# Kernel tuning notes

Measured on AMD Instinct MI355X. Metric: run time of the kernel, lower is better.

Reference implementation:

```python
import jax, jax.numpy as jnp
import numpy as np

N = 50000
E = 400000
F_IN = 128
NUM_CLASSES = 16
# (heads, out_channels, concat) per GATConv layer
LAYERS = [(8, 32, True), (8, 16, True), (8, 8, True), (1, NUM_CLASSES, False)]
DIMS_IN = [F_IN, 256, 128, 64]
NEG_SLOPE = 0.2
BN_EPS = 1e-5


def setup_inputs() -> dict:
    key = jax.random.key(0)
    ks = iter(jax.random.split(key, 64))
    inp = {}
    inp["x"] = jax.random.normal(next(ks), (N, F_IN), dtype=jnp.float32)
    inp["src"] = jax.random.randint(next(ks), (E,), 0, N, dtype=jnp.int32)
    inp["dst"] = jax.random.randint(next(ks), (E,), 0, N, dtype=jnp.int32)
    for l, ((h, c, concat), din) in enumerate(zip(LAYERS, DIMS_IN), start=1):
        s = 1.0 / np.sqrt(din)
        inp[f"W{l}"] = jax.random.normal(next(ks), (din, h * c), dtype=jnp.float32) * s
        inp[f"asrc{l}"] = jax.random.normal(next(ks), (h, c), dtype=jnp.float32) * 0.1
        inp[f"adst{l}"] = jax.random.normal(next(ks), (h, c), dtype=jnp.float32) * 0.1
        dout = h * c if concat else c
        inp[f"b{l}"] = jax.random.normal(next(ks), (dout,), dtype=jnp.float32) * 0.01
        inp[f"g{l}"] = jax.random.uniform(next(ks), (dout,), dtype=jnp.float32, minval=0.5, maxval=1.5)
        inp[f"be{l}"] = jax.random.normal(next(ks), (dout,), dtype=jnp.float32) * 0.1
        inp[f"rm{l}"] = jax.random.normal(next(ks), (dout,), dtype=jnp.float32) * 0.1
        inp[f"rv{l}"] = jax.random.uniform(next(ks), (dout,), dtype=jnp.float32, minval=0.5, maxval=1.5)
    return inp


def _gat_conv(x, src, dst, W, a_src, a_dst, bias, heads, ch, concat):
    n = x.shape[0]
    h = (x @ W).reshape(n, heads, ch)                     # [N,H,C]
    e_s = jnp.einsum('nhc,hc->nh', h, a_src)              # [N,H]
    e_d = jnp.einsum('nhc,hc->nh', h, a_dst)
    alpha = jax.nn.leaky_relu(e_s[src] + e_d[dst], NEG_SLOPE)   # [E,H]
    amax = jax.ops.segment_max(alpha, dst, num_segments=n)
    ex = jnp.exp(alpha - amax[dst])
    den = jax.ops.segment_sum(ex, dst, num_segments=n)
    attn = ex / (den[dst] + 1e-16)                        # [E,H]
    out = jax.ops.segment_sum(h[src] * attn[:, :, None], dst, num_segments=n)  # [N,H,C]
    out = out.reshape(n, heads * ch) if concat else out.mean(axis=1)
    return out + bias


def _bn(x, g, b, rm, rv):
    return (x - rm) * jax.lax.rsqrt(rv + BN_EPS) * g + b


def _forward(x, src, dst, params):
    # PyG GATConv adds self-loops by default
    loops = jnp.arange(N, dtype=src.dtype)
    s = jnp.concatenate([src, loops])
    d = jnp.concatenate([dst, loops])
    out = x
    for l, (h, c, concat) in enumerate(LAYERS, start=1):
        W, a_s, a_d, b, g, be, rm, rv = (params[f"{k}{l}"] for k in
                                         ("W", "asrc", "adst", "b", "g", "be", "rm", "rv"))
        out = _gat_conv(out, s, d, W, a_s, a_d, b, h, c, concat)
        if l < 4:
            out = jax.nn.elu(out)
        out = _bn(out, g, be, rm, rv)
    return out


def reference(x, src, dst,
              W1, asrc1, adst1, b1, g1, be1, rm1, rv1,
              W2, asrc2, adst2, b2, g2, be2, rm2, rv2,
              W3, asrc3, adst3, b3, g3, be3, rm3, rv3,
              W4, asrc4, adst4, b4, g4, be4, rm4, rv4):
    params = dict(
        W1=W1, asrc1=asrc1, adst1=adst1, b1=b1, g1=g1, be1=be1, rm1=rm1, rv1=rv1,
        W2=W2, asrc2=asrc2, adst2=adst2, b2=b2, g2=g2, be2=be2, rm2=rm2, rv2=rv2,
        W3=W3, asrc3=asrc3, adst3=adst3, b3=b3, g3=g3, be3=be3, rm3=rm3, rv3=rv3,
        W4=W4, asrc4=asrc4, adst4=adst4, b4=b4, g4=g4, be4=be4, rm4=rm4, rv4=rv4)
    return _forward(x, src, dst, params)
```

## Files before the change

### kernel.cpp

```cpp
#include <hip/hip_runtime.h>

#define NEG_SLOPE 0.2f
#define BN_EPS 1e-5f

typedef unsigned short u16;
typedef unsigned int u32;
typedef __bf16 bf16x8 __attribute__((ext_vector_type(8)));
typedef float f32x4 __attribute__((ext_vector_type(4)));

__device__ __forceinline__ u32 f2bf(float f) {
    u32 u = __float_as_uint(f);
    return (u + 0x7FFFu + ((u >> 16) & 1u)) >> 16;
}
__device__ __forceinline__ float bf2f(u32 h) { return __uint_as_float(h << 16); }
__device__ __forceinline__ float bfl(u32 p) { return __uint_as_float(p << 16); }
__device__ __forceinline__ float bfh(u32 p) { return __uint_as_float(p & 0xFFFF0000u); }

__global__ void split_kernel(const float4* __restrict__ X, uint2* __restrict__ hi,
                             uint2* __restrict__ lo, int n4) {
    int i = blockIdx.x * blockDim.x + threadIdx.x;
    if (i >= n4) return;
    float4 v = X[i];
    u32 h0 = f2bf(v.x), h1 = f2bf(v.y), h2 = f2bf(v.z), h3 = f2bf(v.w);
    hi[i] = make_uint2(h0 | (h1 << 16), h2 | (h3 << 16));
    u32 l0 = f2bf(v.x - bf2f(h0)), l1 = f2bf(v.y - bf2f(h1)),
        l2 = f2bf(v.z - bf2f(h2)), l3 = f2bf(v.w - bf2f(h3));
    lo[i] = make_uint2(l0 | (l1 << 16), l2 | (l3 << 16));
}

__global__ void wt_prep(const float* __restrict__ W, u16* __restrict__ hi,
                        u16* __restrict__ lo, int K, int N) {
    int i = blockIdx.x * blockDim.x + threadIdx.x;
    if (i >= K * N) return;
    int k = i / N, n = i - k * N;
    float w = W[i];
    u32 h = f2bf(w);
    hi[n * K + k] = (u16)h;
    lo[n * K + k] = (u16)f2bf(w - bf2f(h));
}

__launch_bounds__(256)
__global__ void gemm_mfma(const u16* __restrict__ Ahi, const u16* __restrict__ Alo,
                          const u16* __restrict__ Bhi, const u16* __restrict__ Blo,
                          u16* __restrict__ Cbf, int M, int K, int N) {
    __shared__ uint4 sA[2][512];
    __shared__ uint4 sB[2][512];
    const int tid = threadIdx.x;
    const int bm = blockIdx.y * 128;
    const int bn = blockIdx.x * 128;
    const int lane = tid & 63;
    const int w = tid >> 6;
    const int wm = (w >> 1) * 64;
    const int wn = (w & 1) * 64;
    const int fr = lane & 15;
    const int fs = lane >> 4;
    f32x4 zero = {0.f, 0.f, 0.f, 0.f};
    f32x4 acc[4][4];
    #pragma unroll
    for (int i = 0; i < 4; i++)
        #pragma unroll
        for (int j = 0; j < 4; j++) acc[i][j] = zero;

    const int r0 = tid >> 2;
    const int ss = tid & 3;
    const int r1 = r0 + 64;
    const int d0 = r0 * 4 + (ss ^ ((r0 >> 1) & 3));
    const int d1 = r1 * 4 + (ss ^ ((r1 >> 1) & 3));

    for (int k0 = 0; k0 < K; k0 += 32) {
        {
            int gr = bm + r0;
            uint4 vh = make_uint4(0, 0, 0, 0), vl = make_uint4(0, 0, 0, 0);
            if (gr < M) {
                vh = *(const uint4*)(Ahi + (size_t)gr * K + k0 + ss * 8);
                vl = *(const uint4*)(Alo + (size_t)gr * K + k0 + ss * 8);
            }
            sA[0][d0] = vh; sA[1][d0] = vl;
            gr = bm + r1;
            vh = make_uint4(0, 0, 0, 0); vl = make_uint4(0, 0, 0, 0);
            if (gr < M) {
                vh = *(const uint4*)(Ahi + (size_t)gr * K + k0 + ss * 8);
                vl = *(const uint4*)(Alo + (size_t)gr * K + k0 + ss * 8);
            }
            sA[0][d1] = vh; sA[1][d1] = vl;
        }
        {
            int gr = bn + r0;
            sB[0][d0] = *(const uint4*)(Bhi + (size_t)gr * K + k0 + ss * 8);
            sB[1][d0] = *(const uint4*)(Blo + (size_t)gr * K + k0 + ss * 8);
            gr = bn + r1;
            sB[0][d1] = *(const uint4*)(Bhi + (size_t)gr * K + k0 + ss * 8);
            sB[1][d1] = *(const uint4*)(Blo + (size_t)gr * K + k0 + ss * 8);
        }
        __syncthreads();
        bf16x8 ah[4], al[4], bh[4], bl[4];
        #pragma unroll
        for (int mi = 0; mi < 4; mi++) {
            int row = wm + mi * 16 + fr;
            int idx = row * 4 + (fs ^ ((row >> 1) & 3));
            ah[mi] = *reinterpret_cast<const bf16x8*>(&sA[0][idx]);
            al[mi] = *reinterpret_cast<const bf16x8*>(&sA[1][idx]);
        }
        #pragma unroll
        for (int ni = 0; ni < 4; ni++) {
            int row = wn + ni * 16 + fr;
            int idx = row * 4 + (fs ^ ((row >> 1) & 3));
            bh[ni] = *reinterpret_cast<const bf16x8*>(&sB[0][idx]);
            bl[ni] = *reinterpret_cast<const bf16x8*>(&sB[1][idx]);
        }
        #pragma unroll
        for (int mi = 0; mi < 4; mi++)
            #pragma unroll
            for (int ni = 0; ni < 4; ni++) {
                acc[mi][ni] = __builtin_amdgcn_mfma_f32_16x16x32_bf16(ah[mi], bh[ni], acc[mi][ni], 0, 0, 0);
                acc[mi][ni] = __builtin_amdgcn_mfma_f32_16x16x32_bf16(ah[mi], bl[ni], acc[mi][ni], 0, 0, 0);
                acc[mi][ni] = __builtin_amdgcn_mfma_f32_16x16x32_bf16(al[mi], bh[ni], acc[mi][ni], 0, 0, 0);
            }
        __syncthreads();
    }
    #pragma unroll
    for (int mi = 0; mi < 4; mi++) {
        #pragma unroll
        for (int ni = 0; ni < 4; ni++) {
            int colg = bn + wn + ni * 16 + fr;
            int rbase = bm + wm + mi * 16 + fs * 4;
            #pragma unroll
            for (int r = 0; r < 4; r++) {
                int rw = rbase + r;
                if (rw < M) Cbf[(size_t)rw * N + colg] = (u16)f2bf(acc[mi][ni][r]);
            }
        }
    }
}

template<int TN>
__launch_bounds__(256)
__global__ void gemm_tile(const float* __restrict__ A, const float* __restrict__ B,
                          u16* __restrict__ Cbf, int M, int K, int N) {
    constexpr int BNt = 16 * TN;
    __shared__ float As[32][132];
    __shared__ float Bs[32][BNt + 4];
    const int bm = blockIdx.y * 128;
    const int bn = blockIdx.x * BNt;
    const int tid = threadIdx.x;
    const int tr = tid >> 4;
    const int tc = tid & 15;
    const int la_m = tid >> 3;
    const int la_k = (tid & 7) << 2;
    const int lb_row = tid / (BNt / 4);
    const int lb_c = (tid % (BNt / 4)) * 4;
    float acc[8][TN] = {};
    for (int k0 = 0; k0 < K; k0 += 32) {
        #pragma unroll
        for (int p = 0; p < 4; p++) {
            int m = la_m + p * 32;
            int gm = bm + m;
            float4 v = make_float4(0.f, 0.f, 0.f, 0.f);
            if (gm < M) v = *reinterpret_cast<const float4*>(&A[(size_t)gm * K + k0 + la_k]);
            As[la_k + 0][m] = v.x;
            As[la_k + 1][m] = v.y;
            As[la_k + 2][m] = v.z;
            As[la_k + 3][m] = v.w;
        }
        #pragma unroll
        for (int p = 0; p < BNt / 32; p++) {
            int kk = lb_row + p * (1024 / BNt);
            *reinterpret_cast<float4*>(&Bs[kk][lb_c]) =
                *reinterpret_cast<const float4*>(&B[(size_t)(k0 + kk) * N + bn + lb_c]);
        }
        __syncthreads();
        #pragma unroll
        for (int kk = 0; kk < 32; kk++) {
            float a[8], b[TN];
            float4 a0 = *reinterpret_cast<const float4*>(&As[kk][tr * 4]);
            float4 a1 = *reinterpret_cast<const float4*>(&As[kk][64 + tr * 4]);
            a[0] = a0.x; a[1] = a0.y; a[2] = a0.z; a[3] = a0.w;
            a[4] = a1.x; a[5] = a1.y; a[6] = a1.z; a[7] = a1.w;
            float4 b0 = *reinterpret_cast<const float4*>(&Bs[kk][tc * 4]);
            b[0] = b0.x; b[1] = b0.y; b[2] = b0.z; b[3] = b0.w;
            if constexpr (TN == 8) {
                float4 b1 = *reinterpret_cast<const float4*>(&Bs[kk][64 + tc * 4]);
                b[4] = b1.x; b[5] = b1.y; b[6] = b1.z; b[7] = b1.w;
            }
            #pragma unroll
            for (int i = 0; i < 8; i++)
                #pragma unroll
                for (int j = 0; j < TN; j++)
                    acc[i][j] += a[i] * b[j];
        }
        __syncthreads();
    }
    #pragma unroll
    for (int i = 0; i < 8; i++) {
        int m = bm + ((i < 4) ? (tr * 4 + i) : (64 + tr * 4 + (i - 4)));
        if (m >= M) continue;
        uint2 p0 = make_uint2(f2bf(acc[i][0]) | (f2bf(acc[i][1]) << 16),
                              f2bf(acc[i][2]) | (f2bf(acc[i][3]) << 16));
        *reinterpret_cast<uint2*>(&Cbf[(size_t)m * N + bn + tc * 4]) = p0;
        if constexpr (TN == 8) {
            uint2 p1 = make_uint2(f2bf(acc[i][4]) | (f2bf(acc[i][5]) << 16),
                                  f2bf(acc[i][6]) | (f2bf(acc[i][7]) << 16));
            *reinterpret_cast<uint2*>(&Cbf[(size_t)m * N + bn + 64 + tc * 4]) = p1;
        }
    }
}

__launch_bounds__(256)
__global__ void gemm_k64n16(const float* __restrict__ A, const float* __restrict__ B,
                            u16* __restrict__ Cbf, int M) {
    __shared__ float As[64][68];
    __shared__ float Bs[64][16];
    const int tid = threadIdx.x;
    const int bm = blockIdx.x * 64;
    {
        int r = tid >> 2, c = (tid & 3) << 2;
        *reinterpret_cast<float4*>(&Bs[r][c]) = *reinterpret_cast<const float4*>(&B[r * 16 + c]);
    }
    #pragma unroll
    for (int p = 0; p < 4; p++) {
        int m = (tid >> 4) + p * 16;
        int c = (tid & 15) << 2;
        int gm = bm + m;
        float4 v = make_float4(0.f, 0.f, 0.f, 0.f);
        if (gm < M) v = *reinterpret_cast<const float4*>(&A[(size_t)gm * 64 + c]);
        *reinterpret_cast<float4*>(&As[m][c]) = v;
    }
    __syncthreads();
    const int tc = tid & 15;
    const int r0 = tid >> 4;
    float acc[4] = {};
    #pragma unroll
    for (int k4 = 0; k4 < 16; k4++) {
        float b0 = Bs[4 * k4 + 0][tc];
        float b1 = Bs[4 * k4 + 1][tc];
        float b2 = Bs[4 * k4 + 2][tc];
        float b3 = Bs[4 * k4 + 3][tc];
        #pragma unroll
        for (int i = 0; i < 4; i++) {
            float4 av = *reinterpret_cast<const float4*>(&As[r0 + i * 16][4 * k4]);
            acc[i] += av.x * b0 + av.y * b1 + av.z * b2 + av.w * b3;
        }
    }
    #pragma unroll
    for (int i = 0; i < 4; i++) {
        int m = bm + r0 + i * 16;
        if (m < M) Cbf[(size_t)m * 16 + tc] = (u16)f2bf(acc[i]);
    }
}

__global__ void scores_kernel(const u16* __restrict__ h,
                              const float* __restrict__ asrc,
                              const float* __restrict__ adst,
                              float* __restrict__ es, float* __restrict__ ed,
                              int Nn, int H, int C) {
    int idx = blockIdx.x * blockDim.x + threadIdx.x;
    if (idx >= Nn * H) return;
    int n = idx / H, hh = idx % H;
    const u16* hp = h + ((size_t)n * H + hh) * C;
    const float4* ap = reinterpret_cast<const float4*>(asrc + hh * C);
    const float4* bp = reinterpret_cast<const float4*>(adst + hh * C);
    float s = 0.f, d = 0.f;
    for (int c4 = 0; c4 < C / 4; c4++) {
        uint2 pv = *reinterpret_cast<const uint2*>(hp + 4 * c4);
        float v0 = bfl(pv.x), v1 = bfh(pv.x), v2 = bfl(pv.y), v3 = bfh(pv.y);
        float4 a = ap[c4], b = bp[c4];
        s += v0 * a.x + v1 * a.y + v2 * a.z + v3 * a.w;
        d += v0 * b.x + v1 * b.y + v2 * b.z + v3 * b.w;
    }
    es[idx] = s;
    ed[idx] = d;
}

__global__ void hist_kernel(const int* __restrict__ dst, int* __restrict__ counts,
                            int E0, int Etot) {
    int e = blockIdx.x * blockDim.x + threadIdx.x;
    if (e >= Etot) return;
    int d_ = (e < E0) ? dst[e] : e - E0;
    atomicAdd(&counts[d_], 1);
}

__global__ void scan_kernel(const int* __restrict__ counts, int* __restrict__ row_ptr, int Nn) {
    __shared__ int wsum[16];
    __shared__ int chunk_total;
    __shared__ int carry_s;
    const int tid = threadIdx.x;
    const int lane = tid & 63;
    const int wid = tid >> 6;
    if (tid == 0) carry_s = 0;
    __syncthreads();
    for (int base = 0; base < Nn; base += 1024) {
        int i = base + tid;
        int v = (i < Nn) ? counts[i] : 0;
        int iv = v;
        #pragma unroll
        for (int off = 1; off < 64; off <<= 1) {
            int t = __shfl_up(iv, off, 64);
            if (lane >= off) iv += t;
        }
        if (lane == 63) wsum[wid] = iv;
        __syncthreads();
        if (tid == 0) {
            int s = 0;
            #pragma unroll
            for (int k = 0; k < 16; k++) { int t = wsum[k]; wsum[k] = s; s += t; }
            chunk_total = s;
        }
        __syncthreads();
        if (i < Nn) row_ptr[i] = carry_s + wsum[wid] + (iv - v);
        __syncthreads();
        if (tid == 0) carry_s += chunk_total;
        __syncthreads();
    }
    if (tid == 0) row_ptr[Nn] = carry_s;
}

__global__ void scatter_kernel(const int* __restrict__ src, const int* __restrict__ dst,
                               int* __restrict__ cursor, int* __restrict__ col,
                               int E0, int Etot) {
    int e = blockIdx.x * blockDim.x + threadIdx.x;
    if (e >= Etot) return;
    int d_ = (e < E0) ? dst[e] : e - E0;
    int s_ = (e < E0) ? src[e] : e - E0;
    int pos = atomicAdd(&cursor[d_], 1);
    col[pos] = s_;
}

template<int H, int C, int NT, int DO_ELU>
__launch_bounds__(256)
__global__ void gat_fused(const int* __restrict__ row_ptr, const int* __restrict__ col,
                          const float* __restrict__ es, const float* __restrict__ ed,
                          const u16* __restrict__ h16, float* __restrict__ out,
                          const float* __restrict__ bias, const float* __restrict__ g,
                          const float* __restrict__ be, const float* __restrict__ rm,
                          const float* __restrict__ rv, int Nn) {
    constexpr int Dout = H * C;
    constexpr int VEC = Dout / NT;
    constexpr int NPB = 256 / NT;
    constexpr int CH = 64;
    __shared__ float w_s[NPB][CH][H];
    __shared__ int   c_s[NPB][CH];
    __shared__ float ed_s[NPB][H];
    __shared__ int   md;
    const int tid = threadIdx.x;
    const int slot = tid / NT;
    const int t = tid % NT;
    const int node = blockIdx.x * NPB + slot;
    const bool alive = node < Nn;
    int jb = 0, je = 0;
    if (alive) { jb = row_ptr[node]; je = row_ptr[node + 1]; }
    if (tid == 0) md = 0;
    __syncthreads();
    if (alive && t == 0) atomicMax(&md, je - jb);
    if (alive && t < H) ed_s[slot][t] = ed[node * H + t];
    __syncthreads();
    const int nch = (md + CH - 1) / CH;
    const int c0 = t * VEC;
    const int hh = c0 / C;
    float acc[VEC] = {};
    float den = 0.f;
    for (int cc = 0; cc < nch; cc++) {
        int j0 = jb + cc * CH;
        int cnt = je - j0;
        if (cnt > CH) cnt = CH;
        if (alive) {
            for (int tt = t; tt < cnt; tt += NT) {
                int s = col[j0 + tt];
                c_s[slot][tt] = s;
                if constexpr (H == 8) {
                    const float4* ep = reinterpret_cast<const float4*>(&es[s * 8]);
                    float4 e0 = ep[0], e1 = ep[1];
                    float al[8] = {e0.x, e0.y, e0.z, e0.w, e1.x, e1.y, e1.z, e1.w};
                    #pragma unroll
                    for (int h2 = 0; h2 < 8; h2++) {
                        float a = al[h2] + ed_s[slot][h2];
                        a = (a >= 0.f) ? a : NEG_SLOPE * a;
                        w_s[slot][tt][h2] = __expf(a);
                    }
                } else {
                    float a = es[s] + ed_s[slot][0];
                    a = (a >= 0.f) ? a : NEG_SLOPE * a;
                    w_s[slot][tt][0] = __expf(a);
                }
            }
        }
        __syncthreads();
        if (alive && cnt > 0) {
            int j = 0;
            if constexpr (VEC == 4) {
                for (; j + 4 <= cnt; j += 4) {
                    int s0 = c_s[slot][j],     s1 = c_s[slot][j + 1];
                    int s2 = c_s[slot][j + 2], s3 = c_s[slot][j + 3];
                    float w0 = w_s[slot][j][hh],     w1 = w_s[slot][j + 1][hh];
                    float w2 = w_s[slot][j + 2][hh], w3 = w_s[slot][j + 3][hh];
                    const uint2 p0 = *reinterpret_cast<const uint2*>(h16 + (size_t)s0 * Dout + c0);
                    const uint2 p1 = *reinterpret_cast<const uint2*>(h16 + (size_t)s1 * Dout + c0);
                    const uint2 p2 = *reinterpret_cast<const uint2*>(h16 + (size_t)s2 * Dout + c0);
                    const uint2 p3 = *reinterpret_cast<const uint2*>(h16 + (size_t)s3 * Dout + c0);
                    den += (w0 + w1) + (w2 + w3);
                    acc[0] += w0 * bfl(p0.x) + w1 * bfl(p1.x) + w2 * bfl(p2.x) + w3 * bfl(p3.x);
                    acc[1] += w0 * bfh(p0.x) + w1 * bfh(p1.x) + w2 * bfh(p2.x) + w3 * bfh(p3.x);
                    acc[2] += w0 * bfl(p0.y) + w1 * bfl(p1.y) + w2 * bfl(p2.y) + w3 * bfl(p3.y);
                    acc[3] += w0 * bfh(p0.y) + w1 * bfh(p1.y) + w2 * bfh(p2.y) + w3 * bfh(p3.y);
                }
            } else if constexpr (VEC == 2) {
                for (; j + 4 <= cnt; j += 4) {
                    int s0 = c_s[slot][j],     s1 = c_s[slot][j + 1];
                    int s2 = c_s[slot][j + 2], s3 = c_s[slot][j + 3];
                    float w0 = w_s[slot][j][hh],     w1 = w_s[slot][j + 1][hh];
                    float w2 = w_s[slot][j + 2][hh], w3 = w_s[slot][j + 3][hh];
                    const u32 p0 = *reinterpret_cast<const u32*>(h16 + (size_t)s0 * Dout + c0);
                    const u32 p1 = *reinterpret_cast<const u32*>(h16 + (size_t)s1 * Dout + c0);
                    const u32 p2 = *reinterpret_cast<const u32*>(h16 + (size_t)s2 * Dout + c0);
                    const u32 p3 = *reinterpret_cast<const u32*>(h16 + (size_t)s3 * Dout + c0);
                    den += (w0 + w1) + (w2 + w3);
                    acc[0] += w0 * bfl(p0) + w1 * bfl(p1) + w2 * bfl(p2) + w3 * bfl(p3);
                    acc[1] += w0 * bfh(p0) + w1 * bfh(p1) + w2 * bfh(p2) + w3 * bfh(p3);
                }
            } else {
                for (; j + 4 <= cnt; j += 4) {
                    int s0 = c_s[slot][j],     s1 = c_s[slot][j + 1];
                    int s2 = c_s[slot][j + 2], s3 = c_s[slot][j + 3];
                    float w0 = w_s[slot][j][hh],     w1 = w_s[slot][j + 1][hh];
                    float w2 = w_s[slot][j + 2][hh], w3 = w_s[slot][j + 3][hh];
                    float v0 = bf2f(h16[(size_t)s0 * Dout + c0]);
                    float v1 = bf2f(h16[(size_t)s1 * Dout + c0]);
                    float v2 = bf2f(h16[(size_t)s2 * Dout + c0]);
                    float v3 = bf2f(h16[(size_t)s3 * Dout + c0]);
                    den += (w0 + w1) + (w2 + w3);
                    acc[0] += w0 * v0 + w1 * v1 + w2 * v2 + w3 * v3;
                }
            }
            for (; j < cnt; j++) {
                float w = w_s[slot][j][hh];
                den += w;
                const u16* hp = h16 + (size_t)c_s[slot][j] * Dout + c0;
                if constexpr (VEC == 4) {
                    const uint2 pv = *reinterpret_cast<const uint2*>(hp);
                    acc[0] += w * bfl(pv.x); acc[1] += w * bfh(pv.x);
                    acc[2] += w * bfl(pv.y); acc[3] += w * bfh(pv.y);
                } else if constexpr (VEC == 2) {
                    const u32 pv = *reinterpret_cast<const u32*>(hp);
                    acc[0] += w * bfl(pv); acc[1] += w * bfh(pv);
                } else {
                    acc[0] += w * bf2f(hp[0]);
                }
            }
        }
        __syncthreads();
    }
    if (!alive) return;
    const float inv = 1.f / (den + 1e-16f);
    float res[VEC];
    #pragma unroll
    for (int v = 0; v < VEC; v++) {
        const int jc = c0 + v;
        float y = acc[v] * inv + bias[jc];
        if (DO_ELU) y = (y > 0.f) ? y : expm1f(y);
        y = (y - rm[jc]) * rsqrtf(rv[jc] + BN_EPS) * g[jc] + be[jc];
        res[v] = y;
    }
    float* op = out + (size_t)node * Dout + c0;
    if constexpr (VEC == 4) {
        *reinterpret_cast<float4*>(op) = make_float4(res[0], res[1], res[2], res[3]);
    } else if constexpr (VEC == 2) {
        *reinterpret_cast<float2*>(op) = make_float2(res[0], res[1]);
    } else {
        op[0] = res[0];
    }
}

extern "C" void kernel_launch(void* const* d_in, const int* in_sizes, int n_in,
                              void* d_out, int out_size, void* d_ws, size_t ws_size,
                              hipStream_t stream) {
    const float* x = (const float*)d_in[0];
    const int* src = (const int*)d_in[1];
    const int* dst = (const int*)d_in[2];
    const int Nn = in_sizes[0] / 128;
    const int E0 = in_sizes[1];
    const int Etot = E0 + Nn;

    float* B0 = (float*)d_ws;
    float* B1 = B0 + (size_t)Nn * 256;
    float* es = B1 + (size_t)Nn * 256;
    float* ed = es + (size_t)Nn * 8;
    int* row_ptr = (int*)(ed + (size_t)Nn * 8);
    int* cursor  = row_ptr + (Nn + 1);
    int* col     = cursor + Nn;
    u16* wth = (u16*)(col + Etot);
    u16* wtl = wth + 256 * 256;

    hipMemsetAsync(cursor, 0, sizeof(int) * Nn, stream);
    hist_kernel<<<(Etot + 255) / 256, 256, 0, stream>>>(dst, cursor, E0, Etot);
    scan_kernel<<<1, 1024, 0, stream>>>(cursor, row_ptr, Nn);
    hipMemcpyAsync(cursor, row_ptr, sizeof(int) * Nn, hipMemcpyDeviceToDevice, stream);
    scatter_kernel<<<(Etot + 255) / 256, 256, 0, stream>>>(src, dst, cursor, col, E0, Etot);

    const int gy128 = (Nn + 127) / 128;

    for (int l = 0; l < 4; l++) {
        const float* const* p = (const float* const*)(d_in + 3 + l * 8);
        const float* W    = p[0];
        const float* asrc = p[1];
        const float* adst = p[2];
        const float* bias = p[3];
        const float* g    = p[4];
        const float* be   = p[5];
        const float* rm   = p[6];
        const float* rv   = p[7];

        if (l == 0) {
            const int K = 128, N = 256;
            u16* SH = (u16*)B1;
            u16* SL = SH + (size_t)Nn * K;
            int n4 = Nn * K / 4;
            split_kernel<<<(n4 + 255) / 256, 256, 0, stream>>>(
                (const float4*)x, (uint2*)SH, (uint2*)SL, n4);
            wt_prep<<<(K * N + 255) / 256, 256, 0, stream>>>(W, wth, wtl, K, N);
            u16* h1 = (u16*)B0;
            gemm_mfma<<<dim3(N / 128, gy128), 256, 0, stream>>>(SH, SL, wth, wtl, h1, Nn, K, N);
            scores_kernel<<<(Nn * 8 + 255) / 256, 256, 0, stream>>>(h1, asrc, adst, es, ed, Nn, 8, 32);
            gat_fused<8, 32, 64, 1><<<(Nn + 3) / 4, 256, 0, stream>>>(
                row_ptr, col, es, ed, h1, B1, bias, g, be, rm, rv, Nn);
        } else if (l == 1) {
            const int K = 256, N = 128;
            u16* SH = (u16*)B0;
            u16* SL = SH + (size_t)Nn * K;
            int n4 = Nn * K / 4;
            split_kernel<<<(n4 + 255) / 256, 256, 0, stream>>>(
                (const float4*)B1, (uint2*)SH, (uint2*)SL, n4);
            wt_prep<<<(K * N + 255) / 256, 256, 0, stream>>>(W, wth, wtl, K, N);
            u16* h2 = (u16*)B1;
            float* out2 = B1 + (size_t)Nn * 64;
            gemm_mfma<<<dim3(N / 128, gy128), 256, 0, stream>>>(SH, SL, wth, wtl, h2, Nn, K, N);
            scores_kernel<<<(Nn * 8 + 255) / 256, 256, 0, stream>>>(h2, asrc, adst, es, ed, Nn, 8, 16);
            gat_fused<8, 16, 64, 1><<<(Nn + 3) / 4, 256, 0, stream>>>(
                row_ptr, col, es, ed, h2, out2, bias, g, be, rm, rv, Nn);
        } else if (l == 2) {
            const float* in = B1 + (size_t)Nn * 64;
            u16* h3 = (u16*)B0;
            float* out3 = B0 + (size_t)Nn * 32;
            gemm_tile<4><<<dim3(1, gy128), 256, 0, stream>>>(in, W, h3, Nn, 128, 64);
            scores_kernel<<<(Nn * 8 + 255) / 256, 256, 0, stream>>>(h3, asrc, adst, es, ed, Nn, 8, 8);
            gat_fused<8, 8, 64, 1><<<(Nn + 3) / 4, 256, 0, stream>>>(
                row_ptr, col, es, ed, h3, out3, bias, g, be, rm, rv, Nn);
        } else {
            const float* in = B0 + (size_t)Nn * 32;
            u16* h4 = (u16*)B1;
            gemm_k64n16<<<(Nn + 63) / 64, 256, 0, stream>>>(in, W, h4, Nn);
            scores_kernel<<<(Nn + 255) / 256, 256, 0, stream>>>(h4, asrc, adst, es, ed, Nn, 1, 16);
            gat_fused<1, 16, 16, 0><<<(Nn + 15) / 16, 256, 0, stream>>>(
                row_ptr, col, es, ed, h4, (float*)d_out, bias, g, be, rm, rv, Nn);
        }
    }
}
```

Before: 407.1 us.

## Fuse bf16 hi/lo split into GAT epilogue, use MFMA for layer 3, widen per-thread vectors

The aggregation kernel now writes its outputs directly as bf16 hi/lo pairs, so the separate split pass before the next layer's GEMM is removed. Layer 3 moves from the scalar FP32 tiled GEMM to a BN=64 variant of the MFMA GEMM. The gather kernel gives each thread more features per node (8- or 4-wide loads) and packs more nodes per block. It drops the block-wide max-degree synchronization and __syncthreads, relying on per-wave LDS waits and early exit for dead nodes. This removes barrier stalls and an extra memory pass, at the cost of relying on wave-synchronous behaviour that only holds if each node's threads stay within one wavefront.

```diff
diff --git a/kernel.cpp b/kernel.cpp
--- a/kernel.cpp
+++ b/kernel.cpp
@@ -39,25 +39,27 @@
     lo[n * K + k] = (u16)f2bf(w - bf2f(h));
 }
 
+template<int BN>
 __launch_bounds__(256)
 __global__ void gemm_mfma(const u16* __restrict__ Ahi, const u16* __restrict__ Alo,
                           const u16* __restrict__ Bhi, const u16* __restrict__ Blo,
                           u16* __restrict__ Cbf, int M, int K, int N) {
+    constexpr int FM = (BN == 128) ? 4 : 2;
     __shared__ uint4 sA[2][512];
-    __shared__ uint4 sB[2][512];
+    __shared__ uint4 sB[2][BN * 4];
     const int tid = threadIdx.x;
     const int bm = blockIdx.y * 128;
-    const int bn = blockIdx.x * 128;
+    const int bn = blockIdx.x * BN;
     const int lane = tid & 63;
     const int w = tid >> 6;
-    const int wm = (w >> 1) * 64;
-    const int wn = (w & 1) * 64;
+    const int wm = (BN == 128) ? (w >> 1) * 64 : w * 32;
+    const int wn = (BN == 128) ? (w & 1) * 64 : 0;
     const int fr = lane & 15;
     const int fs = lane >> 4;
     f32x4 zero = {0.f, 0.f, 0.f, 0.f};
-    f32x4 acc[4][4];
-    #pragma unroll
-    for (int i = 0; i < 4; i++)
+    f32x4 acc[FM][4];
+    #pragma unroll
+    for (int i = 0; i < FM; i++)
         #pragma unroll
         for (int j = 0; j < 4; j++) acc[i][j] = zero;
 
@@ -88,14 +90,16 @@
             int gr = bn + r0;
             sB[0][d0] = *(const uint4*)(Bhi + (size_t)gr * K + k0 + ss * 8);
             sB[1][d0] = *(const uint4*)(Blo + (size_t)gr * K + k0 + ss * 8);
-            gr = bn + r1;
-            sB[0][d1] = *(const uint4*)(Bhi + (size_t)gr * K + k0 + ss * 8);
-            sB[1][d1] = *(const uint4*)(Blo + (size_t)gr * K + k0 + ss * 8);
-        }
-        __syncthreads();
-        bf16x8 ah[4], al[4], bh[4], bl[4];
-        #pragma unroll
-        for (int mi = 0; mi < 4; mi++) {
+            if constexpr (BN == 128) {
+                gr = bn + r1;
+                sB[0][d1] = *(const uint4*)(Bhi + (size_t)gr * K + k0 + ss * 8);
+                sB[1][d1] = *(const uint4*)(Blo + (size_t)gr * K + k0 + ss * 8);
+            }
+        }
+        __syncthreads();
+        bf16x8 ah[FM], al[FM], bh[4], bl[4];
+        #pragma unroll
+        for (int mi = 0; mi < FM; mi++) {
             int row = wm + mi * 16 + fr;
             int idx = row * 4 + (fs ^ ((row >> 1) & 3));
             ah[mi] = *reinterpret_cast<const bf16x8*>(&sA[0][idx]);
@@ -109,7 +113,7 @@
             bl[ni] = *reinterpret_cast<const bf16x8*>(&sB[1][idx]);
         }
         #pragma unroll
-        for (int mi = 0; mi < 4; mi++)
+        for (int mi = 0; mi < FM; mi++)
             #pragma unroll
             for (int ni = 0; ni < 4; ni++) {
                 acc[mi][ni] = __builtin_amdgcn_mfma_f32_16x16x32_bf16(ah[mi], bh[ni], acc[mi][ni], 0, 0, 0);
@@ -119,7 +123,7 @@
         __syncthreads();
     }
     #pragma unroll
-    for (int mi = 0; mi < 4; mi++) {
+    for (int mi = 0; mi < FM; mi++) {
         #pragma unroll
         for (int ni = 0; ni < 4; ni++) {
             int colg = bn + wn + ni * 16 + fr;
@@ -129,78 +133,6 @@
                 int rw = rbase + r;
                 if (rw < M) Cbf[(size_t)rw * N + colg] = (u16)f2bf(acc[mi][ni][r]);
             }
-        }
-    }
-}
-
-template<int TN>
-__launch_bounds__(256)
-__global__ void gemm_tile(const float* __restrict__ A, const float* __restrict__ B,
-                          u16* __restrict__ Cbf, int M, int K, int N) {
-    constexpr int BNt = 16 * TN;
-    __shared__ float As[32][132];
-    __shared__ float Bs[32][BNt + 4];
-    const int bm = blockIdx.y * 128;
-    const int bn = blockIdx.x * BNt;
-    const int tid = threadIdx.x;
-    const int tr = tid >> 4;
-    const int tc = tid & 15;
-    const int la_m = tid >> 3;
-    const int la_k = (tid & 7) << 2;
-    const int lb_row = tid / (BNt / 4);
-    const int lb_c = (tid % (BNt / 4)) * 4;
-    float acc[8][TN] = {};
-    for (int k0 = 0; k0 < K; k0 += 32) {
-        #pragma unroll
-        for (int p = 0; p < 4; p++) {
-            int m = la_m + p * 32;
-            int gm = bm + m;
-            float4 v = make_float4(0.f, 0.f, 0.f, 0.f);
-            if (gm < M) v = *reinterpret_cast<const float4*>(&A[(size_t)gm * K + k0 + la_k]);
-            As[la_k + 0][m] = v.x;
-            As[la_k + 1][m] = v.y;
-            As[la_k + 2][m] = v.z;
-            As[la_k + 3][m] = v.w;
-        }
-        #pragma unroll
-        for (int p = 0; p < BNt / 32; p++) {
-            int kk = lb_row + p * (1024 / BNt);
-            *reinterpret_cast<float4*>(&Bs[kk][lb_c]) =
-                *reinterpret_cast<const float4*>(&B[(size_t)(k0 + kk) * N + bn + lb_c]);
-        }
-        __syncthreads();
-        #pragma unroll
-        for (int kk = 0; kk < 32; kk++) {
-            float a[8], b[TN];
-            float4 a0 = *reinterpret_cast<const float4*>(&As[kk][tr * 4]);
-            float4 a1 = *reinterpret_cast<const float4*>(&As[kk][64 + tr * 4]);
-            a[0] = a0.x; a[1] = a0.y; a[2] = a0.z; a[3] = a0.w;
-            a[4] = a1.x; a[5] = a1.y; a[6] = a1.z; a[7] = a1.w;
-            float4 b0 = *reinterpret_cast<const float4*>(&Bs[kk][tc * 4]);
-            b[0] = b0.x; b[1] = b0.y; b[2] = b0.z; b[3] = b0.w;
-            if constexpr (TN == 8) {
-                float4 b1 = *reinterpret_cast<const float4*>(&Bs[kk][64 + tc * 4]);
-                b[4] = b1.x; b[5] = b1.y; b[6] = b1.z; b[7] = b1.w;
-            }
-            #pragma unroll
-            for (int i = 0; i < 8; i++)
-                #pragma unroll
-                for (int j = 0; j < TN; j++)
-                    acc[i][j] += a[i] * b[j];
-        }
-        __syncthreads();
-    }
-    #pragma unroll
-    for (int i = 0; i < 8; i++) {
-        int m = bm + ((i < 4) ? (tr * 4 + i) : (64 + tr * 4 + (i - 4)));
-        if (m >= M) continue;
-        uint2 p0 = make_uint2(f2bf(acc[i][0]) | (f2bf(acc[i][1]) << 16),
-                              f2bf(acc[i][2]) | (f2bf(acc[i][3]) << 16));
-        *reinterpret_cast<uint2*>(&Cbf[(size_t)m * N + bn + tc * 4]) = p0;
-        if constexpr (TN == 8) {
-            uint2 p1 = make_uint2(f2bf(acc[i][4]) | (f2bf(acc[i][5]) << 16),
-                                  f2bf(acc[i][6]) | (f2bf(acc[i][7]) << 16));
-            *reinterpret_cast<uint2*>(&Cbf[(size_t)m * N + bn + 64 + tc * 4]) = p1;
         }
     }
 }
@@ -325,130 +257,112 @@
     col[pos] = s_;
 }
 
-template<int H, int C, int NT, int DO_ELU>
+template<int H, int C, int NT, int DO_ELU, int OUT_HILO>
 __launch_bounds__(256)
 __global__ void gat_fused(const int* __restrict__ row_ptr, const int* __restrict__ col,
                           const float* __restrict__ es, const float* __restrict__ ed,
-                          const u16* __restrict__ h16, float* __restrict__ out,
+                          const u16* __restrict__ h16, float* __restrict__ outf,
+                          u16* __restrict__ outh, u16* __restrict__ outl,
                           const float* __restrict__ bias, const float* __restrict__ g,
                           const float* __restrict__ be, const float* __restrict__ rm,
                           const float* __restrict__ rv, int Nn) {
     constexpr int Dout = H * C;
     constexpr int VEC = Dout / NT;
     constexpr int NPB = 256 / NT;
-    constexpr int CH = 64;
+    constexpr int CH = 32;
     __shared__ float w_s[NPB][CH][H];
     __shared__ int   c_s[NPB][CH];
-    __shared__ float ed_s[NPB][H];
-    __shared__ int   md;
     const int tid = threadIdx.x;
     const int slot = tid / NT;
     const int t = tid % NT;
     const int node = blockIdx.x * NPB + slot;
-    const bool alive = node < Nn;
-    int jb = 0, je = 0;
-    if (alive) { jb = row_ptr[node]; je = row_ptr[node + 1]; }
-    if (tid == 0) md = 0;
-    __syncthreads();
-    if (alive && t == 0) atomicMax(&md, je - jb);
-    if (alive && t < H) ed_s[slot][t] = ed[node * H + t];
-    __syncthreads();
-    const int nch = (md + CH - 1) / CH;
+    if (node >= Nn) return;
+    const int jb = row_ptr[node], je = row_ptr[node + 1];
+    float edv[H];
+    if constexpr (H == 8) {
+        float4 e0 = *reinterpret_cast<const float4*>(&ed[node * 8]);
+        float4 e1 = *reinterpret_cast<const float4*>(&ed[node * 8 + 4]);
+        edv[0] = e0.x; edv[1] = e0.y; edv[2] = e0.z; edv[3] = e0.w;
+        edv[4] = e1.x; edv[5] = e1.y; edv[6] = e1.z; edv[7] = e1.w;
+    } else {
+        edv[0] = ed[node];
+    }
     const int c0 = t * VEC;
     const int hh = c0 / C;
     float acc[VEC] = {};
     float den = 0.f;
-    for (int cc = 0; cc < nch; cc++) {
-        int j0 = jb + cc * CH;
+    for (int j0 = jb; j0 < je; j0 += CH) {
         int cnt = je - j0;
         if (cnt > CH) cnt = CH;
-        if (alive) {
-            for (int tt = t; tt < cnt; tt += NT) {
-                int s = col[j0 + tt];
-                c_s[slot][tt] = s;
-                if constexpr (H == 8) {
-                    const float4* ep = reinterpret_cast<const float4*>(&es[s * 8]);
-                    float4 e0 = ep[0], e1 = ep[1];
-                    float al[8] = {e0.x, e0.y, e0.z, e0.w, e1.x, e1.y, e1.z, e1.w};
-                    #pragma unroll
-                    for (int h2 = 0; h2 < 8; h2++) {
-                        float a = al[h2] + ed_s[slot][h2];
-                        a = (a >= 0.f) ? a : NEG_SLOPE * a;
-                        w_s[slot][tt][h2] = __expf(a);
-                    }
-                } else {
-                    float a = es[s] + ed_s[slot][0];
+        for (int tt = t; tt < cnt; tt += NT) {
+            int s = col[j0 + tt];
+            c_s[slot][tt] = s;
+            if constexpr (H == 8) {
+                float4 q0 = *reinterpret_cast<const float4*>(&es[s * 8]);
+                float4 q1 = *reinterpret_cast<const float4*>(&es[s * 8 + 4]);
+                float al8[8] = {q0.x, q0.y, q0.z, q0.w, q1.x, q1.y, q1.z, q1.w};
+                #pragma unroll
+                for (int h2 = 0; h2 < 8; h2++) {
+                    float a = al8[h2] + edv[h2];
                     a = (a >= 0.f) ? a : NEG_SLOPE * a;
-                    w_s[slot][tt][0] = __expf(a);
-                }
-            }
-        }
-        __syncthreads();
-        if (alive && cnt > 0) {
-            int j = 0;
-            if constexpr (VEC == 4) {
-                for (; j + 4 <= cnt; j += 4) {
-                    int s0 = c_s[slot][j],     s1 = c_s[slot][j + 1];
-                    int s2 = c_s[slot][j + 2], s3 = c_s[slot][j + 3];
-                    float w0 = w_s[slot][j][hh],     w1 = w_s[slot][j + 1][hh];
-                    float w2 = w_s[slot][j + 2][hh], w3 = w_s[slot][j + 3][hh];
-                    const uint2 p0 = *reinterpret_cast<const uint2*>(h16 + (size_t)s0 * Dout + c0);
-                    const uint2 p1 = *reinterpret_cast<const uint2*>(h16 + (size_t)s1 * Dout + c0);
-                    const uint2 p2 = *reinterpret_cast<const uint2*>(h16 + (size_t)s2 * Dout + c0);
-                    const uint2 p3 = *reinterpret_cast<const uint2*>(h16 + (size_t)s3 * Dout + c0);
-                    den += (w0 + w1) + (w2 + w3);
-                    acc[0] += w0 * bfl(p0.x) + w1 * bfl(p1.x) + w2 * bfl(p2.x) + w3 * bfl(p3.x);
-                    acc[1] += w0 * bfh(p0.x) + w1 * bfh(p1.x) + w2 * bfh(p2.x) + w3 * bfh(p3.x);
-                    acc[2] += w0 * bfl(p0.y) + w1 * bfl(p1.y) + w2 * bfl(p2.y) + w3 * bfl(p3.y);
-                    acc[3] += w0 * bfh(p0.y) + w1 * bfh(p1.y) + w2 * bfh(p2.y) + w3 * bfh(p3.y);
-                }
-            } else if constexpr (VEC == 2) {
-                for (; j + 4 <= cnt; j += 4) {
-                    int s0 = c_s[slot][j],     s1 = c_s[slot][j + 1];
-                    int s2 = c_s[slot][j + 2], s3 = c_s[slot][j + 3];
-                    float w0 = w_s[slot][j][hh],     w1 = w_s[slot][j + 1][hh];
-                    float w2 = w_s[slot][j + 2][hh], w3 = w_s[slot][j + 3][hh];
-                    const u32 p0 = *reinterpret_cast<const u32*>(h16 + (size_t)s0 * Dout + c0);
-                    const u32 p1 = *reinterpret_cast<const u32*>(h16 + (size_t)s1 * Dout + c0);
-                    const u32 p2 = *reinterpret_cast<const u32*>(h16 + (size_t)s2 * Dout + c0);
-                    const u32 p3 = *reinterpret_cast<const u32*>(h16 + (size_t)s3 * Dout + c0);
-                    den += (w0 + w1) + (w2 + w3);
-                    acc[0] += w0 * bfl(p0) + w1 * bfl(p1) + w2 * bfl(p2) + w3 * bfl(p3);
-                    acc[1] += w0 * bfh(p0) + w1 * bfh(p1) + w2 * bfh(p2) + w3 * bfh(p3);
+                    w_s[slot][tt][h2] = __expf(a);
                 }
             } else {
-                for (; j + 4 <= cnt; j += 4) {
-                    int s0 = c_s[slot][j],     s1 = c_s[slot][j + 1];
-                    int s2 = c_s[slot][j + 2], s3 = c_s[slot][j + 3];
-                    float w0 = w_s[slot][j][hh],     w1 = w_s[slot][j + 1][hh];
-                    float w2 = w_s[slot][j + 2][hh], w3 = w_s[slot][j + 3][hh];
-                    float v0 = bf2f(h16[(size_t)s0 * Dout + c0]);
-                    float v1 = bf2f(h16[(size_t)s1 * Dout + c0]);
-                    float v2 = bf2f(h16[(size_t)s2 * Dout + c0]);
-                    float v3 = bf2f(h16[(size_t)s3 * Dout + c0]);
-                    den += (w0 + w1) + (w2 + w3);
-                    acc[0] += w0 * v0 + w1 * v1 + w2 * v2 + w3 * v3;
+                float a = es[s] + edv[0];
+                a = (a >= 0.f) ? a : NEG_SLOPE * a;
+                w_s[slot][tt][0] = __expf(a);
+            }
+        }
+        asm volatile("s_waitcnt lgkmcnt(0)" ::: "memory");
+        int j = 0;
+        for (; j + 4 <= cnt; j += 4) {
+            int sx[4]; float ww[4];
+            #pragma unroll
+            for (int u = 0; u < 4; u++) { sx[u] = c_s[slot][j + u]; ww[u] = w_s[slot][j + u][hh]; }
+            if constexpr (VEC == 8) {
+                uint4 pv[4];
+                #pragma unroll
+                for (int u = 0; u < 4; u++)
+                    pv[u] = *reinterpret_cast<const uint4*>(h16 + (size_t)sx[u] * Dout + c0);
+                #pragma unroll
+                for (int u = 0; u < 4; u++) {
+                    den += ww[u];
+                    acc[0] += ww[u] * bfl(pv[u].x); acc[1] += ww[u] * bfh(pv[u].x);
+                    acc[2] += ww[u] * bfl(pv[u].y); acc[3] += ww[u] * bfh(pv[u].y);
+                    acc[4] += ww[u] * bfl(pv[u].z); acc[5] += ww[u] * bfh(pv[u].z);
+                    acc[6] += ww[u] * bfl(pv[u].w); acc[7] += ww[u] * bfh(pv[u].w);
                 }
-            }
-            for (; j < cnt; j++) {
-                float w = w_s[slot][j][hh];
-                den += w;
-                const u16* hp = h16 + (size_t)c_s[slot][j] * Dout + c0;
-                if constexpr (VEC == 4) {
-                    const uint2 pv = *reinterpret_cast<const uint2*>(hp);
-                    acc[0] += w * bfl(pv.x); acc[1] += w * bfh(pv.x);
-                    acc[2] += w * bfl(pv.y); acc[3] += w * bfh(pv.y);
-                } else if constexpr (VEC == 2) {
-                    const u32 pv = *reinterpret_cast<const u32*>(hp);
-                    acc[0] += w * bfl(pv); acc[1] += w * bfh(pv);
-                } else {
-                    acc[0] += w * bf2f(hp[0]);
+            } else {
+                uint2 pv[4];
+                #pragma unroll
+                for (int u = 0; u < 4; u++)
+                    pv[u] = *reinterpret_cast<const uint2*>(h16 + (size_t)sx[u] * Dout + c0);
+                #pragma unroll
+                for (int u = 0; u < 4; u++) {
+                    den += ww[u];
+                    acc[0] += ww[u] * bfl(pv[u].x); acc[1] += ww[u] * bfh(pv[u].x);
+                    acc[2] += ww[u] * bfl(pv[u].y); acc[3] += ww[u] * bfh(pv[u].y);
                 }
             }
         }
-        __syncthreads();
-    }
-    if (!alive) return;
+        for (; j < cnt; j++) {
+            float w = w_s[slot][j][hh];
+            den += w;
+            const u16* hp = h16 + (size_t)c_s[slot][j] * Dout + c0;
+            if constexpr (VEC == 8) {
+                uint4 pv = *reinterpret_cast<const uint4*>(hp);
+                acc[0] += w * bfl(pv.x); acc[1] += w * bfh(pv.x);
+                acc[2] += w * bfl(pv.y); acc[3] += w * bfh(pv.y);
+                acc[4] += w * bfl(pv.z); acc[5] += w * bfh(pv.z);
+                acc[6] += w * bfl(pv.w); acc[7] += w * bfh(pv.w);
+            } else {
+                uint2 pv = *reinterpret_cast<const uint2*>(hp);
+                acc[0] += w * bfl(pv.x); acc[1] += w * bfh(pv.x);
+                acc[2] += w * bfl(pv.y); acc[3] += w * bfh(pv.y);
+            }
+        }
+        asm volatile("s_waitcnt lgkmcnt(0)" ::: "memory");
+    }
     const float inv = 1.f / (den + 1e-16f);
     float res[VEC];
     #pragma unroll
@@ -459,13 +373,34 @@
         y = (y - rm[jc]) * rsqrtf(rv[jc] + BN_EPS) * g[jc] + be[jc];
         res[v] = y;
     }
-    float* op = out + (size_t)node * Dout + c0;
-    if constexpr (VEC == 4) {
-        *reinterpret_cast<float4*>(op) = make_float4(res[0], res[1], res[2], res[3]);
-    } else if constexpr (VEC == 2) {
-        *reinterpret_cast<float2*>(op) = make_float2(res[0], res[1]);
+    if constexpr (OUT_HILO) {
+        u32 rh[VEC], rl[VEC];
+        #pragma unroll
+        for (int v = 0; v < VEC; v++) {
+            rh[v] = f2bf(res[v]);
+            rl[v] = f2bf(res[v] - bf2f(rh[v]));
+        }
+        if constexpr (VEC == 8) {
+            uint4 ph = make_uint4(rh[0] | (rh[1] << 16), rh[2] | (rh[3] << 16),
+                                  rh[4] | (rh[5] << 16), rh[6] | (rh[7] << 16));
+            uint4 pl = make_uint4(rl[0] | (rl[1] << 16), rl[2] | (rl[3] << 16),
+                                  rl[4] | (rl[5] << 16), rl[6] | (rl[7] << 16));
+            *reinterpret_cast<uint4*>(outh + (size_t)node * Dout + c0) = ph;
+            *reinterpret_cast<uint4*>(outl + (size_t)node * Dout + c0) = pl;
+        } else {
+            uint2 ph = make_uint2(rh[0] | (rh[1] << 16), rh[2] | (rh[3] << 16));
+            uint2 pl = make_uint2(rl[0] | (rl[1] << 16), rl[2] | (rl[3] << 16));
+            *reinterpret_cast<uint2*>(outh + (size_t)node * Dout + c0) = ph;
+            *reinterpret_cast<uint2*>(outl + (size_t)node * Dout + c0) = pl;
+        }
     } else {
-        op[0] = res[0];
+        float* op = outf + (size_t)node * Dout + c0;
+        if constexpr (VEC == 8) {
+            *reinterpret_cast<float4*>(op) = make_float4(res[0], res[1], res[2], res[3]);
+            *reinterpret_cast<float4*>(op + 4) = make_float4(res[4], res[5], res[6], res[7]);
+        } else {
+            *reinterpret_cast<float4*>(op) = make_float4(res[0], res[1], res[2], res[3]);
+        }
     }
 }
 
@@ -479,15 +414,24 @@
     const int E0 = in_sizes[1];
     const int Etot = E0 + Nn;
 
-    float* B0 = (float*)d_ws;
-    float* B1 = B0 + (size_t)Nn * 256;
-    float* es = B1 + (size_t)Nn * 256;
+    u16* A0 = (u16*)d_ws;
+    u16* Bh = A0 + (size_t)Nn * 512;
+    u16* Ch = Bh + (size_t)Nn * 256;
+    float* es = (float*)(Ch + (size_t)Nn * 256);
     float* ed = es + (size_t)Nn * 8;
     int* row_ptr = (int*)(ed + (size_t)Nn * 8);
     int* cursor  = row_ptr + (Nn + 1);
     int* col     = cursor + Nn;
     u16* wth = (u16*)(col + Etot);
-    u16* wtl = wth + 256 * 256;
+    u16* wtl = wth + 65536;
+
+    u16* XH = A0;
+    u16* XL = A0 + (size_t)Nn * 128;
+    u16* Y1H = A0;
+    u16* Y1L = A0 + (size_t)Nn * 256;
+    u16* Y2H = Ch;
+    u16* Y2L = Ch + (size_t)Nn * 128;
+    float* out3 = (float*)A0;
 
     hipMemsetAsync(cursor, 0, sizeof(int) * Nn, stream);
     hist_kernel<<<(Etot + 255) / 256, 256, 0, stream>>>(dst, cursor, E0, Etot);
@@ -510,46 +454,33 @@
 
         if (l == 0) {
             const int K = 128, N = 256;
-            u16* SH = (u16*)B1;
-            u16* SL = SH + (size_t)Nn * K;
             int n4 = Nn * K / 4;
             split_kernel<<<(n4 + 255) / 256, 256, 0, stream>>>(
-                (const float4*)x, (uint2*)SH, (uint2*)SL, n4);
+                (const float4*)x, (uint2*)XH, (uint2*)XL, n4);
             wt_prep<<<(K * N + 255) / 256, 256, 0, stream>>>(W, wth, wtl, K, N);
-            u16* h1 = (u16*)B0;
-            gemm_mfma<<<dim3(N / 128, gy128), 256, 0, stream>>>(SH, SL, wth, wtl, h1, Nn, K, N);
-            scores_kernel<<<(Nn * 8 + 255) / 256, 256, 0, stream>>>(h1, asrc, adst, es, ed, Nn, 8, 32);
-            gat_fused<8, 32, 64, 1><<<(Nn + 3) / 4, 256, 0, stream>>>(
-                row_ptr, col, es, ed, h1, B1, bias, g, be, rm, rv, Nn);
+            gemm_mfma<128><<<dim3(N / 128, gy128), 256, 0, stream>>>(XH, XL, wth, wtl, Bh, Nn, K, N);
+            scores_kernel<<<(Nn * 8 + 255) / 256, 256, 0, stream>>>(Bh, asrc, adst, es, ed, Nn, 8, 32);
+            gat_fused<8, 32, 32, 1, 1><<<(Nn + 7) / 8, 256, 0, stream>>>(
+                row_ptr, col, es, ed, Bh, nullptr, Y1H, Y1L, bias, g, be, rm, rv, Nn);
         } else if (l == 1) {
             const int K = 256, N = 128;
-            u16* SH = (u16*)B0;
-            u16* SL = SH + (size_t)Nn * K;
-            int n4 = Nn * K / 4;
-            split_kernel<<<(n4 + 255) / 256, 256, 0, stream>>>(
-                (const float4*)B1, (uint2*)SH, (uint2*)SL, n4);
             wt_prep<<<(K * N + 255) / 256, 256, 0, stream>>>(W, wth, wtl, K, N);
-            u16* h2 = (u16*)B1;
-            float* out2 = B1 + (size_t)Nn * 64;
-            gemm_mfma<<<dim3(N / 128, gy128), 256, 0, stream>>>(SH, SL, wth, wtl, h2, Nn, K, N);
-            scores_kernel<<<(Nn * 8 + 255) / 256, 256, 0, stream>>>(h2, asrc, adst, es, ed, Nn, 8, 16);
-            gat_fused<8, 16, 64, 1><<<(Nn + 3) / 4, 256, 0, stream>>>(
-                row_ptr, col, es, ed, h2, out2, bias, g, be, rm, rv, Nn);
+            gemm_mfma<128><<<dim3(1, gy128), 256, 0, stream>>>(Y1H, Y1L, wth, wtl, Bh, Nn, K, N);
+            scores_kernel<<<(Nn * 8 + 255) / 256, 256, 0, stream>>>(Bh, asrc, adst, es, ed, Nn, 8, 16);
+            gat_fused<8, 16, 16, 1, 1><<<(Nn + 15) / 16, 256, 0, stream>>>(
+                row_ptr, col, es, ed, Bh, nullptr, Y2H, Y2L, bias, g, be, rm, rv, Nn);
         } else if (l == 2) {
-            const float* in = B1 + (size_t)Nn * 64;
-            u16* h3 = (u16*)B0;
-            float* out3 = B0 + (size_t)Nn * 32;
-            gemm_tile<4><<<dim3(1, gy128), 256, 0, stream>>>(in, W, h3, Nn, 128, 64);
-            scores_kernel<<<(Nn * 8 + 255) / 256, 256, 0, stream>>>(h3, asrc, adst, es, ed, Nn, 8, 8);
-            gat_fused<8, 8, 64, 1><<<(Nn + 3) / 4, 256, 0, stream>>>(
-                row_ptr, col, es, ed, h3, out3, bias, g, be, rm, rv, Nn);
+            const int K = 128, N = 64;
+            wt_prep<<<(K * N + 255) / 256, 256, 0, stream>>>(W, wth, wtl, K, N);
+            gemm_mfma<64><<<dim3(1, gy128), 256, 0, stream>>>(Y2H, Y2L, wth, wtl, Bh, Nn, K, N);
+            scores_kernel<<<(Nn * 8 + 255) / 256, 256, 0, stream>>>(Bh, asrc, adst, es, ed, Nn, 8, 8);
+            gat_fused<8, 8, 16, 1, 0><<<(Nn + 15) / 16, 256, 0, stream>>>(
+                row_ptr, col, es, ed, Bh, out3, nullptr, nullptr, bias, g, be, rm, rv, Nn);
         } else {
-            const float* in = B0 + (size_t)Nn * 32;
-            u16* h4 = (u16*)B1;
-            gemm_k64n16<<<(Nn + 63) / 64, 256, 0, stream>>>(in, W, h4, Nn);
-            scores_kernel<<<(Nn + 255) / 256, 256, 0, stream>>>(h4, asrc, adst, es, ed, Nn, 1, 16);
-            gat_fused<1, 16, 16, 0><<<(Nn + 15) / 16, 256, 0, stream>>>(
-                row_ptr, col, es, ed, h4, (float*)d_out, bias, g, be, rm, rv, Nn);
-        }
-    }
-}
+            gemm_k64n16<<<(Nn + 63) / 64, 256, 0, stream>>>(out3, W, Bh, Nn);
+            scores_kernel<<<(Nn + 255) / 256, 256, 0, stream>>>(Bh, asrc, adst, es, ed, Nn, 1, 16);
+            gat_fused<1, 16, 4, 0, 0><<<(Nn + 63) / 64, 256, 0, stream>>>(
+                row_ptr, col, es, ed, Bh, (float*)d_out, nullptr, nullptr, bias, g, be, rm, rv, Nn);
+        }
+    }
+}
```

Result: slower. 458.6 us (+12.6%).
